# Optimization experiments

Hardware: AMD Instinct MI355X
Metric: run time of the kernel (lower is better)

Reference implementation:

```python
import jax, jax.numpy as jnp
import numpy as np

N_NODES = 100000
N_EDGES = 1600000
D = 128
BETA = 0.001
EPS = 1e-12  # F.normalize eps


def setup_inputs() -> dict:
    key = jax.random.key(0)
    k1, k2, k3, k4, k5, k6 = jax.random.split(key, 6)
    stdv = 1.0 / np.sqrt(D)
    return {
        "input": jax.random.normal(k1, (N_NODES, D), dtype=jnp.float32),
        "edge_rows": jax.random.randint(k2, (N_EDGES,), 0, N_NODES, dtype=jnp.int32),
        "edge_cols": jax.random.randint(k3, (N_EDGES,), 0, N_NODES, dtype=jnp.int32),
        "edge_vals": jax.random.uniform(k4, (N_EDGES,), dtype=jnp.float32),
        "weight": jax.random.uniform(k5, (D, D), minval=-stdv, maxval=stdv, dtype=jnp.float32),
        "bias": jax.random.uniform(k6, (D,), minval=-stdv, maxval=stdv, dtype=jnp.float32),
    }


def reference(input, edge_rows, edge_cols, edge_vals, weight, bias):
    # dense projection: [N, D]
    support = input @ weight
    # sparse neighbor aggregation: agg[i] = sum_{(i,j) in E} adj_val * support[j]
    msgs = edge_vals[:, None] * support[edge_cols]          # [E, D]
    agg = jax.ops.segment_sum(msgs, edge_rows, num_segments=input.shape[0])
    # beta-weighted residual blend
    out = BETA * input + (1.0 - BETA) * agg
    # row-wise L2 normalize (torch F.normalize, p=2, dim=1)
    norm = jnp.sqrt(jnp.sum(out * out, axis=1, keepdims=True))
    out = out / jnp.maximum(norm, EPS)
    # bias add
    return out + bias
```

## Files before the change

kernel.cpp:

```cpp
#include <hip/hip_runtime.h>

#define N_NODES 100000
#define N_EDGES 1600000
#define D 128
#define NB 1563
#define NSUB 16
#define SUBCAP 128
#define CAP (NSUB*SUBCAP)
#define EPT 8

typedef short bf16x8 __attribute__((ext_vector_type(8)));
typedef float f32x4 __attribute__((ext_vector_type(4)));

__device__ __forceinline__ unsigned short f2bf(float x){
  union { float f; unsigned u; } v; v.f = x;
  unsigned r = v.u + 0x7fffu + ((v.u >> 16) & 1u);
  return (unsigned short)(r >> 16);
}

__device__ __forceinline__ float bf2f(unsigned short h){
  union { unsigned u; float f; } v; v.u = ((unsigned)h) << 16;
  return v.f;
}

__global__ __launch_bounds__(256) void convert_input(const float4* __restrict__ in4,
                                                     ushort4* __restrict__ outb,
                                                     int* __restrict__ cursor,
                                                     const float* __restrict__ W,
                                                     unsigned short* __restrict__ WT){
  int i = blockIdx.x*256 + threadIdx.x;
  if (i < NSUB*NB) cursor[i] = 0;
  if (i < D*D){
    int k = i >> 7, c = i & 127;
    WT[c*128 + k] = f2bf(W[i]);
  }
  float4 a = in4[i];
  ushort4 h;
  h.x = f2bf(a.x); h.y = f2bf(a.y); h.z = f2bf(a.z); h.w = f2bf(a.w);
  outb[i] = h;
}

__global__ __launch_bounds__(256) void scatter_direct(const int4* __restrict__ rows4,
                                                      const int4* __restrict__ cols4,
                                                      const float4* __restrict__ vals4,
                                                      int* __restrict__ cursor,
                                                      int2* __restrict__ edges_s){
  int tid = blockIdx.x*256 + threadIdx.x;
  int base = tid * EPT;
  int s = blockIdx.x & (NSUB-1);
  if (base + EPT <= N_EDGES){
    int4 r0 = rows4[tid*2+0], r1 = rows4[tid*2+1];
    int4 c0 = cols4[tid*2+0], c1 = cols4[tid*2+1];
    float4 v0 = vals4[tid*2+0], v1 = vals4[tid*2+1];
    int r[EPT] = {r0.x, r0.y, r0.z, r0.w, r1.x, r1.y, r1.z, r1.w};
    int c[EPT] = {c0.x, c0.y, c0.z, c0.w, c1.x, c1.y, c1.z, c1.w};
    float v[EPT] = {v0.x, v0.y, v0.z, v0.w, v1.x, v1.y, v1.z, v1.w};
    int pos[EPT];
    #pragma unroll
    for (int k = 0; k < EPT; ++k){
      int b = r[k] >> 6;
      pos[k] = atomicAdd(&cursor[s*NB + b], 1);
    }
    #pragma unroll
    for (int k = 0; k < EPT; ++k){
      int b = r[k] >> 6;
      if (pos[k] < SUBCAP)
        edges_s[(size_t)b*CAP + s*SUBCAP + pos[k]] =
            make_int2(c[k] | ((r[k] & 63) << 17), __float_as_int(v[k]));
    }
  } else {
    const int* rows = (const int*)rows4;
    const int* cols = (const int*)cols4;
    const float* vals = (const float*)vals4;
    for (int k = 0; k < EPT; ++k){
      int i = base + k;
      if (i >= N_EDGES) break;
      int r = rows[i];
      int b = r >> 6;
      int pos = atomicAdd(&cursor[s*NB + b], 1);
      if (pos < SUBCAP)
        edges_s[(size_t)b*CAP + s*SUBCAP + pos] =
            make_int2(cols[i] | ((r & 63) << 17), __float_as_int(vals[i]));
    }
  }
}

__global__ __launch_bounds__(512) void agg_final(const ushort4* __restrict__ inb4,
                                                 const int* __restrict__ cursor,
                                                 const int2* __restrict__ edges_g,
                                                 const ushort4* __restrict__ WT4,
                                                 const float* __restrict__ bias,
                                                 float* __restrict__ out){
  __shared__ unsigned short As[64*136];
  __shared__ unsigned short Ws[128*136];
  __shared__ int hist[64];
  __shared__ int cur[64];
  __shared__ int rs[64];
  __shared__ int rc[64];
  int2* st = (int2*)As;

  int t = threadIdx.x;
  int b = blockIdx.x;
  size_t base = (size_t)b * CAP;

  if (t < 64) hist[t] = 0;
  __syncthreads();

  #pragma unroll
  for (int i = 0; i < 8; ++i){
    int idx4 = i*512 + t;
    int c = idx4 >> 5, k4 = idx4 & 31;
    ushort4 w = WT4[idx4];
    *((ushort4*)&Ws[c*136 + k4*4]) = w;
  }

  int slot = t & 127;
  int sg = t >> 7;
  int2 held[4];
  int hv = 0;
  #pragma unroll
  for (int ss = 0; ss < 4; ++ss){
    int s = sg*4 + ss;
    int ms = cursor[s*NB + b];
    if (ms > SUBCAP) ms = SUBCAP;
    if (slot < ms){
      int2 e = edges_g[base + s*SUBCAP + slot];
      held[ss] = e;
      hv |= (1 << ss);
      atomicAdd(&hist[((unsigned)e.x) >> 17], 1);
    }
  }
  __syncthreads();

  if (t < 64){
    int c = hist[t];
    int x = c;
    #pragma unroll
    for (int o = 1; o < 64; o <<= 1){
      int y = __shfl_up(x, o);
      if (t >= o) x += y;
    }
    int excl = x - c;
    cur[t] = excl;
    rs[t] = excl;
    rc[t] = c;
  }
  __syncthreads();

  #pragma unroll
  for (int ss = 0; ss < 4; ++ss){
    if (hv & (1 << ss)){
      int2 e = held[ss];
      int r = ((unsigned)e.x) >> 17;
      int pos = atomicAdd(&cur[r], 1);
      st[pos] = make_int2(e.x & 0x1FFFF, e.y);
    }
  }
  __syncthreads();

  int grp = t >> 5, l = t & 31;
  float4 res[4];
  #pragma unroll
  for (int j = 0; j < 4; ++j){
    int r = grp*4 + j;
    int e = rs[r], end = e + rc[r];
    float4 a0 = make_float4(0.f,0.f,0.f,0.f);
    float4 a1 = make_float4(0.f,0.f,0.f,0.f);
    float4 a2 = make_float4(0.f,0.f,0.f,0.f);
    float4 a3 = make_float4(0.f,0.f,0.f,0.f);
    for (; e + 4 <= end; e += 4){
      int2 e0 = st[e+0];
      int2 e1 = st[e+1];
      int2 e2 = st[e+2];
      int2 e3 = st[e+3];
      ushort4 x0 = inb4[(size_t)e0.x*32 + l];
      ushort4 x1 = inb4[(size_t)e1.x*32 + l];
      ushort4 x2 = inb4[(size_t)e2.x*32 + l];
      ushort4 x3 = inb4[(size_t)e3.x*32 + l];
      float v0 = __int_as_float(e0.y), v1 = __int_as_float(e1.y);
      float v2 = __int_as_float(e2.y), v3 = __int_as_float(e3.y);
      a0.x = fmaf(v0, bf2f(x0.x), a0.x); a0.y = fmaf(v0, bf2f(x0.y), a0.y);
      a0.z = fmaf(v0, bf2f(x0.z), a0.z); a0.w = fmaf(v0, bf2f(x0.w), a0.w);
      a1.x = fmaf(v1, bf2f(x1.x), a1.x); a1.y = fmaf(v1, bf2f(x1.y), a1.y);
      a1.z = fmaf(v1, bf2f(x1.z), a1.z); a1.w = fmaf(v1, bf2f(x1.w), a1.w);
      a2.x = fmaf(v2, bf2f(x2.x), a2.x); a2.y = fmaf(v2, bf2f(x2.y), a2.y);
      a2.z = fmaf(v2, bf2f(x2.z), a2.z); a2.w = fmaf(v2, bf2f(x2.w), a2.w);
      a3.x = fmaf(v3, bf2f(x3.x), a3.x); a3.y = fmaf(v3, bf2f(x3.y), a3.y);
      a3.z = fmaf(v3, bf2f(x3.z), a3.z); a3.w = fmaf(v3, bf2f(x3.w), a3.w);
    }
    for (; e < end; ++e){
      int2 ee = st[e];
      ushort4 x = inb4[(size_t)ee.x*32 + l];
      float v = __int_as_float(ee.y);
      a0.x = fmaf(v, bf2f(x.x), a0.x); a0.y = fmaf(v, bf2f(x.y), a0.y);
      a0.z = fmaf(v, bf2f(x.z), a0.z); a0.w = fmaf(v, bf2f(x.w), a0.w);
    }
    res[j].x = (a0.x + a1.x) + (a2.x + a3.x);
    res[j].y = (a0.y + a1.y) + (a2.y + a3.y);
    res[j].z = (a0.z + a1.z) + (a2.z + a3.z);
    res[j].w = (a0.w + a1.w) + (a2.w + a3.w);
  }
  __syncthreads();

  #pragma unroll
  for (int j = 0; j < 4; ++j){
    int r = grp*4 + j;
    ushort4 h;
    h.x = f2bf(res[j].x); h.y = f2bf(res[j].y);
    h.z = f2bf(res[j].z); h.w = f2bf(res[j].w);
    *((ushort4*)&As[r*136 + l*4]) = h;
  }
  __syncthreads();

  if (t < 256){
    const unsigned short* inb = (const unsigned short*)inb4;
    int block_row = b * 64;
    int wave = t >> 6, lane = t & 63;
    int q = lane >> 4, n = lane & 15;

    bf16x8 afr[4];
    #pragma unroll
    for (int ks = 0; ks < 4; ++ks)
      afr[ks] = *((const bf16x8*)&As[(wave*16 + n)*136 + ks*32 + q*8]);

    f32x4 acc[8];
    #pragma unroll
    for (int ct = 0; ct < 8; ++ct) acc[ct] = (f32x4){0.f, 0.f, 0.f, 0.f};

    #pragma unroll
    for (int ct = 0; ct < 8; ++ct){
      #pragma unroll
      for (int ks = 0; ks < 4; ++ks){
        bf16x8 bfr = *((const bf16x8*)&Ws[(ct*16 + n)*136 + ks*32 + q*8]);
        acc[ct] = __builtin_amdgcn_mfma_f32_16x16x32_bf16(afr[ks], bfr, acc[ct], 0, 0, 0);
      }
    }

    int base_row = block_row + wave*16 + q*4;
    float v[8][4];
    float s[4] = {0.f, 0.f, 0.f, 0.f};
    #pragma unroll
    for (int reg = 0; reg < 4; ++reg){
      int grow = base_row + reg;
      const unsigned short* inrow = inb + (size_t)grow * D;
      #pragma unroll
      for (int ct = 0; ct < 8; ++ct){
        float inp = (grow < N_NODES) ? bf2f(inrow[ct*16 + n]) : 0.f;
        float val = fmaf(0.999f, acc[ct][reg], 0.001f * inp);
        v[ct][reg] = val;
        s[reg] = fmaf(val, val, s[reg]);
      }
    }
    #pragma unroll
    for (int reg = 0; reg < 4; ++reg){
      float x = s[reg];
      x += __shfl_xor(x, 1);
      x += __shfl_xor(x, 2);
      x += __shfl_xor(x, 4);
      x += __shfl_xor(x, 8);
      s[reg] = x;
    }
    #pragma unroll
    for (int reg = 0; reg < 4; ++reg){
      int grow = base_row + reg;
      if (grow >= N_NODES) continue;
      float scale = 1.f / fmaxf(sqrtf(s[reg]), 1e-12f);
      float* outrow = out + (size_t)grow * D;
      #pragma unroll
      for (int ct = 0; ct < 8; ++ct){
        outrow[ct*16 + n] = fmaf(v[ct][reg], scale, bias[ct*16 + n]);
      }
    }
  }
}

extern "C" void kernel_launch(void* const* d_in, const int* in_sizes, int n_in,
                              void* d_out, int out_size, void* d_ws, size_t ws_size,
                              hipStream_t stream){
  const float* input  = (const float*)d_in[0];
  const int*   erows  = (const int*)d_in[1];
  const int*   ecols  = (const int*)d_in[2];
  const float* evals  = (const float*)d_in[3];
  const float* weight = (const float*)d_in[4];
  const float* bias   = (const float*)d_in[5];
  float* out = (float*)d_out;

  int*   cursor    = (int*)d_ws;
  int2*  edges_s   = (int2*)(cursor + NSUB*NB);
  ushort4* inb     = (ushort4*)(edges_s + (size_t)NB*CAP);
  unsigned short* WTg = (unsigned short*)(inb + (size_t)N_NODES * 32);

  convert_input<<<12500, 256, 0, stream>>>((const float4*)input, inb, cursor, weight, WTg);
  int sc_blocks = (N_EDGES + 256*EPT - 1) / (256*EPT);
  scatter_direct<<<sc_blocks, 256, 0, stream>>>((const int4*)erows, (const int4*)ecols,
                                                (const float4*)evals, cursor, edges_s);
  agg_final<<<NB, 512, 0, stream>>>((const ushort4*)inb, cursor, edges_s,
                                    (const ushort4*)WTg, bias, out);
}
```

Before: 314.8 us.

## Fuse convert and scatter kernels, drop W smem staging, restructure edge buckets

Merges the input/weight conversion and the edge scatter into one launch with block-range dispatch, and zeroes the cursor with a memset instead. The sub-bucket layout changes from 16x128 to 8x224 so each thread holds up to 8 edges. The aggregation kernel no longer stages W in shared memory and reads B fragments straight from global memory. It also stages the bf16 input rows into shared memory with coalesced loads for the residual term. The aim is less launch overhead, lower LDS use for better occupancy, and coalesced input reads. The cost is uncached global reads of W inside the MFMA loop and more scattered writes from fewer sub-buckets.

Result: no change. 318.3 us (+1.1%).

```diff
diff --git a/kernel.cpp b/kernel.cpp
--- a/kernel.cpp
+++ b/kernel.cpp
@@ -4,10 +4,11 @@
 #define N_EDGES 1600000
 #define D 128
 #define NB 1563
-#define NSUB 16
-#define SUBCAP 128
+#define NSUB 8
+#define SUBCAP 224
 #define CAP (NSUB*SUBCAP)
 #define EPT 8
+#define SC_BLOCKS 782
 
 typedef short bf16x8 __attribute__((ext_vector_type(8)));
 typedef float f32x4 __attribute__((ext_vector_type(4)));
@@ -23,76 +24,73 @@
   return v.f;
 }
 
-__global__ __launch_bounds__(256) void convert_input(const float4* __restrict__ in4,
-                                                     ushort4* __restrict__ outb,
-                                                     int* __restrict__ cursor,
-                                                     const float* __restrict__ W,
-                                                     unsigned short* __restrict__ WT){
-  int i = blockIdx.x*256 + threadIdx.x;
-  if (i < NSUB*NB) cursor[i] = 0;
-  if (i < D*D){
-    int k = i >> 7, c = i & 127;
-    WT[c*128 + k] = f2bf(W[i]);
-  }
-  float4 a = in4[i];
-  ushort4 h;
-  h.x = f2bf(a.x); h.y = f2bf(a.y); h.z = f2bf(a.z); h.w = f2bf(a.w);
-  outb[i] = h;
-}
-
-__global__ __launch_bounds__(256) void scatter_direct(const int4* __restrict__ rows4,
-                                                      const int4* __restrict__ cols4,
-                                                      const float4* __restrict__ vals4,
-                                                      int* __restrict__ cursor,
-                                                      int2* __restrict__ edges_s){
-  int tid = blockIdx.x*256 + threadIdx.x;
-  int base = tid * EPT;
-  int s = blockIdx.x & (NSUB-1);
-  if (base + EPT <= N_EDGES){
-    int4 r0 = rows4[tid*2+0], r1 = rows4[tid*2+1];
-    int4 c0 = cols4[tid*2+0], c1 = cols4[tid*2+1];
-    float4 v0 = vals4[tid*2+0], v1 = vals4[tid*2+1];
-    int r[EPT] = {r0.x, r0.y, r0.z, r0.w, r1.x, r1.y, r1.z, r1.w};
-    int c[EPT] = {c0.x, c0.y, c0.z, c0.w, c1.x, c1.y, c1.z, c1.w};
-    float v[EPT] = {v0.x, v0.y, v0.z, v0.w, v1.x, v1.y, v1.z, v1.w};
-    int pos[EPT];
-    #pragma unroll
-    for (int k = 0; k < EPT; ++k){
-      int b = r[k] >> 6;
-      pos[k] = atomicAdd(&cursor[s*NB + b], 1);
-    }
-    #pragma unroll
-    for (int k = 0; k < EPT; ++k){
-      int b = r[k] >> 6;
-      if (pos[k] < SUBCAP)
-        edges_s[(size_t)b*CAP + s*SUBCAP + pos[k]] =
-            make_int2(c[k] | ((r[k] & 63) << 17), __float_as_int(v[k]));
+__global__ __launch_bounds__(256) void convert_scatter(
+    const float4* __restrict__ in4, ushort4* __restrict__ outb,
+    const float* __restrict__ W, unsigned short* __restrict__ WT,
+    const int4* __restrict__ rows4, const int4* __restrict__ cols4,
+    const float4* __restrict__ vals4,
+    int* __restrict__ cursor, int2* __restrict__ edges_s){
+  int blk = blockIdx.x;
+  if (blk < SC_BLOCKS){
+    int tid = blk*256 + threadIdx.x;
+    int base = tid * EPT;
+    int s = blk & (NSUB-1);
+    if (base + EPT <= N_EDGES){
+      int4 r0 = rows4[tid*2+0], r1 = rows4[tid*2+1];
+      int4 c0 = cols4[tid*2+0], c1 = cols4[tid*2+1];
+      float4 v0 = vals4[tid*2+0], v1 = vals4[tid*2+1];
+      int r[EPT] = {r0.x, r0.y, r0.z, r0.w, r1.x, r1.y, r1.z, r1.w};
+      int c[EPT] = {c0.x, c0.y, c0.z, c0.w, c1.x, c1.y, c1.z, c1.w};
+      float v[EPT] = {v0.x, v0.y, v0.z, v0.w, v1.x, v1.y, v1.z, v1.w};
+      int pos[EPT];
+      #pragma unroll
+      for (int k = 0; k < EPT; ++k){
+        int b = r[k] >> 6;
+        pos[k] = atomicAdd(&cursor[s*NB + b], 1);
+      }
+      #pragma unroll
+      for (int k = 0; k < EPT; ++k){
+        int b = r[k] >> 6;
+        if (pos[k] < SUBCAP)
+          edges_s[(size_t)b*CAP + s*SUBCAP + pos[k]] =
+              make_int2(c[k] | ((r[k] & 63) << 17), __float_as_int(v[k]));
+      }
+    } else {
+      const int* rows = (const int*)rows4;
+      const int* cols = (const int*)cols4;
+      const float* vals = (const float*)vals4;
+      for (int k = 0; k < EPT; ++k){
+        int i = base + k;
+        if (i >= N_EDGES) break;
+        int r = rows[i];
+        int b = r >> 6;
+        int pos = atomicAdd(&cursor[s*NB + b], 1);
+        if (pos < SUBCAP)
+          edges_s[(size_t)b*CAP + s*SUBCAP + pos] =
+              make_int2(cols[i] | ((r & 63) << 17), __float_as_int(vals[i]));
+      }
     }
   } else {
-    const int* rows = (const int*)rows4;
-    const int* cols = (const int*)cols4;
-    const float* vals = (const float*)vals4;
-    for (int k = 0; k < EPT; ++k){
-      int i = base + k;
-      if (i >= N_EDGES) break;
-      int r = rows[i];
-      int b = r >> 6;
-      int pos = atomicAdd(&cursor[s*NB + b], 1);
-      if (pos < SUBCAP)
-        edges_s[(size_t)b*CAP + s*SUBCAP + pos] =
-            make_int2(cols[i] | ((r & 63) << 17), __float_as_int(vals[i]));
-    }
+    int cb = blk - SC_BLOCKS;
+    int i = cb*256 + threadIdx.x;
+    if (i < D*D){
+      int k = i >> 7, c = i & 127;
+      WT[c*128 + k] = f2bf(W[i]);
+    }
+    float4 a = in4[i];
+    ushort4 h;
+    h.x = f2bf(a.x); h.y = f2bf(a.y); h.z = f2bf(a.z); h.w = f2bf(a.w);
+    outb[i] = h;
   }
 }
 
 __global__ __launch_bounds__(512) void agg_final(const ushort4* __restrict__ inb4,
                                                  const int* __restrict__ cursor,
                                                  const int2* __restrict__ edges_g,
-                                                 const ushort4* __restrict__ WT4,
+                                                 const unsigned short* __restrict__ WTg,
                                                  const float* __restrict__ bias,
                                                  float* __restrict__ out){
   __shared__ unsigned short As[64*136];
-  __shared__ unsigned short Ws[128*136];
   __shared__ int hist[64];
   __shared__ int cur[64];
   __shared__ int rs[64];
@@ -106,27 +104,16 @@
   if (t < 64) hist[t] = 0;
   __syncthreads();
 
-  #pragma unroll
-  for (int i = 0; i < 8; ++i){
-    int idx4 = i*512 + t;
-    int c = idx4 >> 5, k4 = idx4 & 31;
-    ushort4 w = WT4[idx4];
-    *((ushort4*)&Ws[c*136 + k4*4]) = w;
-  }
-
-  int slot = t & 127;
-  int sg = t >> 7;
-  int2 held[4];
+  int2 held[NSUB];
   int hv = 0;
   #pragma unroll
-  for (int ss = 0; ss < 4; ++ss){
-    int s = sg*4 + ss;
+  for (int s = 0; s < NSUB; ++s){
     int ms = cursor[s*NB + b];
     if (ms > SUBCAP) ms = SUBCAP;
-    if (slot < ms){
-      int2 e = edges_g[base + s*SUBCAP + slot];
-      held[ss] = e;
-      hv |= (1 << ss);
+    if (t < ms){
+      int2 e = edges_g[base + s*SUBCAP + t];
+      held[s] = e;
+      hv |= (1 << s);
       atomicAdd(&hist[((unsigned)e.x) >> 17], 1);
     }
   }
@@ -148,9 +135,9 @@
   __syncthreads();
 
   #pragma unroll
-  for (int ss = 0; ss < 4; ++ss){
-    if (hv & (1 << ss)){
-      int2 e = held[ss];
+  for (int s = 0; s < NSUB; ++s){
+    if (hv & (1 << s)){
+      int2 e = held[s];
       int r = ((unsigned)e.x) >> 17;
       int pos = atomicAdd(&cur[r], 1);
       st[pos] = make_int2(e.x & 0x1FFFF, e.y);
@@ -212,64 +199,74 @@
   }
   __syncthreads();
 
+  int wave = t >> 6, lane = t & 63;
+  int q = lane >> 4, n = lane & 15;
+  bf16x8 afr[4];
   if (t < 256){
-    const unsigned short* inb = (const unsigned short*)inb4;
-    int block_row = b * 64;
-    int wave = t >> 6, lane = t & 63;
-    int q = lane >> 4, n = lane & 15;
-
-    bf16x8 afr[4];
     #pragma unroll
     for (int ks = 0; ks < 4; ++ks)
       afr[ks] = *((const bf16x8*)&As[(wave*16 + n)*136 + ks*32 + q*8]);
-
-    f32x4 acc[8];
-    #pragma unroll
-    for (int ct = 0; ct < 8; ++ct) acc[ct] = (f32x4){0.f, 0.f, 0.f, 0.f};
-
+  }
+  __syncthreads();
+
+  int block_row = b * 64;
+  #pragma unroll
+  for (int i = 0; i < 4; ++i){
+    int idx4 = i*512 + t;
+    int row = idx4 >> 5, k4 = idx4 & 31;
+    int grow = block_row + row;
+    ushort4 h = make_ushort4(0,0,0,0);
+    if (grow < N_NODES) h = inb4[(size_t)grow*32 + k4];
+    *((ushort4*)&As[row*136 + k4*4]) = h;
+  }
+  __syncthreads();
+  if (t >= 256) return;
+
+  f32x4 acc[8];
+  #pragma unroll
+  for (int ct = 0; ct < 8; ++ct) acc[ct] = (f32x4){0.f, 0.f, 0.f, 0.f};
+
+  #pragma unroll
+  for (int ct = 0; ct < 8; ++ct){
+    #pragma unroll
+    for (int ks = 0; ks < 4; ++ks){
+      bf16x8 bfr = *((const bf16x8*)(WTg + (ct*16 + n)*128 + ks*32 + q*8));
+      acc[ct] = __builtin_amdgcn_mfma_f32_16x16x32_bf16(afr[ks], bfr, acc[ct], 0, 0, 0);
+    }
+  }
+
+  int base_row = block_row + wave*16 + q*4;
+  float v[8][4];
+  float s[4] = {0.f, 0.f, 0.f, 0.f};
+  #pragma unroll
+  for (int reg = 0; reg < 4; ++reg){
+    int row_local = wave*16 + q*4 + reg;
     #pragma unroll
     for (int ct = 0; ct < 8; ++ct){
-      #pragma unroll
-      for (int ks = 0; ks < 4; ++ks){
-        bf16x8 bfr = *((const bf16x8*)&Ws[(ct*16 + n)*136 + ks*32 + q*8]);
-        acc[ct] = __builtin_amdgcn_mfma_f32_16x16x32_bf16(afr[ks], bfr, acc[ct], 0, 0, 0);
-      }
-    }
-
-    int base_row = block_row + wave*16 + q*4;
-    float v[8][4];
-    float s[4] = {0.f, 0.f, 0.f, 0.f};
-    #pragma unroll
-    for (int reg = 0; reg < 4; ++reg){
-      int grow = base_row + reg;
-      const unsigned short* inrow = inb + (size_t)grow * D;
-      #pragma unroll
-      for (int ct = 0; ct < 8; ++ct){
-        float inp = (grow < N_NODES) ? bf2f(inrow[ct*16 + n]) : 0.f;
-        float val = fmaf(0.999f, acc[ct][reg], 0.001f * inp);
-        v[ct][reg] = val;
-        s[reg] = fmaf(val, val, s[reg]);
-      }
-    }
-    #pragma unroll
-    for (int reg = 0; reg < 4; ++reg){
-      float x = s[reg];
-      x += __shfl_xor(x, 1);
-      x += __shfl_xor(x, 2);
-      x += __shfl_xor(x, 4);
-      x += __shfl_xor(x, 8);
-      s[reg] = x;
-    }
-    #pragma unroll
-    for (int reg = 0; reg < 4; ++reg){
-      int grow = base_row + reg;
-      if (grow >= N_NODES) continue;
-      float scale = 1.f / fmaxf(sqrtf(s[reg]), 1e-12f);
-      float* outrow = out + (size_t)grow * D;
-      #pragma unroll
-      for (int ct = 0; ct < 8; ++ct){
-        outrow[ct*16 + n] = fmaf(v[ct][reg], scale, bias[ct*16 + n]);
-      }
+      float inp = bf2f(As[row_local*136 + ct*16 + n]);
+      float val = fmaf(0.999f, acc[ct][reg], 0.001f * inp);
+      v[ct][reg] = val;
+      s[reg] = fmaf(val, val, s[reg]);
+    }
+  }
+  #pragma unroll
+  for (int reg = 0; reg < 4; ++reg){
+    float x = s[reg];
+    x += __shfl_xor(x, 1);
+    x += __shfl_xor(x, 2);
+    x += __shfl_xor(x, 4);
+    x += __shfl_xor(x, 8);
+    s[reg] = x;
+  }
+  #pragma unroll
+  for (int reg = 0; reg < 4; ++reg){
+    int grow = base_row + reg;
+    if (grow >= N_NODES) continue;
+    float scale = 1.f / fmaxf(sqrtf(s[reg]), 1e-12f);
+    float* outrow = out + (size_t)grow * D;
+    #pragma unroll
+    for (int ct = 0; ct < 8; ++ct){
+      outrow[ct*16 + n] = fmaf(v[ct][reg], scale, bias[ct*16 + n]);
     }
   }
 }
@@ -290,10 +287,11 @@
   ushort4* inb     = (ushort4*)(edges_s + (size_t)NB*CAP);
   unsigned short* WTg = (unsigned short*)(inb + (size_t)N_NODES * 32);
 
-  convert_input<<<12500, 256, 0, stream>>>((const float4*)input, inb, cursor, weight, WTg);
-  int sc_blocks = (N_EDGES + 256*EPT - 1) / (256*EPT);
-  scatter_direct<<<sc_blocks, 256, 0, stream>>>((const int4*)erows, (const int4*)ecols,
-                                                (const float4*)evals, cursor, edges_s);
+  hipMemsetAsync(cursor, 0, NSUB * NB * sizeof(int), stream);
+  convert_scatter<<<SC_BLOCKS + 12500, 256, 0, stream>>>(
+      (const float4*)input, inb, weight, WTg,
+      (const int4*)erows, (const int4*)ecols, (const float4*)evals,
+      cursor, edges_s);
   agg_final<<<NB, 512, 0, stream>>>((const ushort4*)inb, cursor, edges_s,
-                                    (const ushort4*)WTg, bias, out);
-}
+                                    WTg, bias, out);
+}
```
